# Kernel tuning notes

Hardware: AMD Instinct MI355X
Metric: run time of the kernel (lower is better)

The kernel has to match this reference:

```python
import jax, jax.numpy as jnp
import numpy as np
import math

D_MODEL = 1024
NUM_HEADS = 16
HEAD_DIM = D_MODEL // NUM_HEADS
ROPE_THETA = 10000.0
MAX_SEQ_LEN = 4096


def setup_inputs() -> dict:
    key = jax.random.key(0)
    ks = jax.random.split(key, 6)
    sigma = math.sqrt(2.0 / (D_MODEL + D_MODEL))
    def w(k):
        # trunc_normal within [-3sigma, 3sigma] ~ approximate with clipped normal
        return jnp.clip(sigma * jax.random.normal(k, (D_MODEL, D_MODEL), dtype=jnp.float32), -3 * sigma, 3 * sigma)
    x = jax.random.normal(ks[0], (2, 2048, D_MODEL), dtype=jnp.float32)
    token_positions = jnp.arange(2048, dtype=jnp.int64 if jax.config.jax_enable_x64 else jnp.int32)
    return {
        "x": x,
        "wq": w(ks[1]),
        "wk": w(ks[2]),
        "wv": w(ks[3]),
        "wo": w(ks[4]),
        "token_positions": token_positions,
    }


def _rope(t, positions):
    # t: (B, H, S, head_dim); positions: (S,)
    half = HEAD_DIM // 2
    inv_freq = 1.0 / (ROPE_THETA ** (jnp.arange(0, HEAD_DIM, 2, dtype=jnp.float32) / HEAD_DIM))  # (half,)
    freqs = positions.astype(jnp.float32)[:, None] * inv_freq[None, :]  # (S, half)
    cos = jnp.cos(freqs)
    sin = jnp.sin(freqs)
    t_even = t[..., ::2]   # (B,H,S,half)
    t_odd = t[..., 1::2]
    rot_even = t_even * cos - t_odd * sin
    rot_odd = t_even * sin + t_odd * cos
    return jnp.stack([rot_even, rot_odd], axis=-1).reshape(t.shape)


def reference(x, wq, wk, wv, wo, token_positions):
    B, S, _ = x.shape
    def split_heads(t):
        return t.reshape(B, S, NUM_HEADS, HEAD_DIM).transpose(0, 2, 1, 3)  # (B,H,S,Dh)
    q = split_heads(jnp.einsum('bsd,ed->bse', x, wq))
    k = split_heads(jnp.einsum('bsd,ed->bse', x, wk))
    v = split_heads(jnp.einsum('bsd,ed->bse', x, wv))
    q = _rope(q, token_positions)
    k = _rope(k, token_positions)
    scores = jnp.einsum('bhqd,bhkd->bhqk', q, k) / math.sqrt(HEAD_DIM)
    causal = jnp.tril(jnp.ones((S, S), dtype=bool))
    scores = jnp.where(causal, scores, -jnp.inf)
    probs = jax.nn.softmax(scores, axis=-1)
    out = jnp.einsum('bhqk,bhkd->bhqd', probs, v)  # (B,H,S,Dh)
    out = out.transpose(0, 2, 1, 3).reshape(B, S, D_MODEL)
    return jnp.einsum('bsd,ed->bse', out, wo)
```

## Files before the change

### kernel.cpp

```cpp
#include <hip/hip_runtime.h>
#include <hip/hip_bf16.h>


#define D_MODEL 1024
#define NHEADS  16
#define HDIM    64
#define SEQ     2048
#define BATCH   2

typedef unsigned short u16;
typedef __bf16 bf16x8_t __attribute__((ext_vector_type(8)));
typedef float  f32x4_t  __attribute__((ext_vector_type(4)));

__device__ __forceinline__ u16 f2bf(float f) {
    union { __hip_bfloat16 h; u16 u; } cv;
    cv.h = __float2bfloat16(f);
    return cv.u;
}

__device__ __forceinline__ unsigned pk2(float x, float y) {
    union { __hip_bfloat162 h; unsigned u; } cv;
    cv.h = __float22bfloat162_rn(make_float2(x, y));
    return cv.u;
}

__device__ __forceinline__ uint4 pack8(float4 a, float4 b) {
    uint4 u;
    u.x = pk2(a.x, a.y);
    u.y = pk2(a.z, a.w);
    u.z = pk2(b.x, b.y);
    u.w = pk2(b.z, b.w);
    return u;
}

__device__ __forceinline__ bf16x8_t frag_ld(const u16* p) {
    union { uint4 u; bf16x8_t v; } t;
    t.u = *(const uint4*)p;
    return t.v;
}

__device__ __forceinline__ void acc8(uint4 u, float* a) {
    a[0] += __uint_as_float(u.x << 16); a[1] += __uint_as_float(u.x & 0xffff0000u);
    a[2] += __uint_as_float(u.y << 16); a[3] += __uint_as_float(u.y & 0xffff0000u);
    a[4] += __uint_as_float(u.z << 16); a[5] += __uint_as_float(u.z & 0xffff0000u);
    a[6] += __uint_as_float(u.w << 16); a[7] += __uint_as_float(u.w & 0xffff0000u);
}

__device__ __forceinline__ void dma16(const u16* g, u16* l) {
    __builtin_amdgcn_global_load_lds(
        (const __attribute__((address_space(1))) void*)g,
        (__attribute__((address_space(3))) void*)l, 16, 0, 0);
}

__global__ __launch_bounds__(256) void conv_bf16_kernel(
    const float* __restrict__ X, const float* __restrict__ Wq,
    const float* __restrict__ Wk, const float* __restrict__ Wv,
    const float* __restrict__ Wo, u16* __restrict__ Xbf, u16* __restrict__ Wbf)
{
    const size_t gid = (size_t)blockIdx.x * 256 + threadIdx.x;
    const float* src;
    u16* dst;
    size_t off;
    if (gid < (1u << 19)) {
        src = X; dst = Xbf; off = gid;
    } else {
        size_t g = gid - (1u << 19);
        const int wsel = (int)(g >> 17);
        g &= (1u << 17) - 1;
        src = (wsel == 0) ? Wq : (wsel == 1) ? Wk : (wsel == 2) ? Wv : Wo;
        dst = Wbf + ((size_t)wsel << 20);
        off = g;
    }
    const float4 a = *(const float4*)(src + off * 8);
    const float4 b = *(const float4*)(src + off * 8 + 4);
    *(uint4*)(dst + off * 8) = pack8(a, b);
}

__global__ __launch_bounds__(256) void qkv_rope_kernel(
    const u16* __restrict__ Xbf, const u16* __restrict__ Wbf,
    const int* __restrict__ pos,
    u16* __restrict__ Qo, u16* __restrict__ Ko, u16* __restrict__ Vt)
{
    __shared__ __align__(16) u16 smem[16896];
    u16* As = smem;
    u16* Bs = smem + 8192;

    const int tid = threadIdx.x;
    const int m0 = blockIdx.y * 128;
    const int nv = blockIdx.x * 128;
    const int which = nv >> 10;
    const int nbase = nv & 1023;
    const u16* __restrict__ Wsrc = Wbf + ((size_t)which << 20);

    const int w = tid >> 6, L = tid & 63, quad = L >> 4, colL = L & 15;
    const int mw = (w & 1) * 64, nw = (w >> 1) * 64;

    const int lrow = L >> 3;
    const int lchk = (L & 7) ^ lrow;
    const u16* ag = Xbf + (size_t)(m0 + 32 * w + lrow) * D_MODEL + lchk * 8;
    const u16* bg = Wsrc + (size_t)(nbase + 32 * w + lrow) * D_MODEL + lchk * 8;
    u16* al = As + (32 * w) * 64;
    u16* bl = Bs + (32 * w) * 64;

    f32x4_t acc[4][4];
    #pragma unroll
    for (int i = 0; i < 4; ++i)
        #pragma unroll
        for (int j = 0; j < 4; ++j) acc[i][j] = (f32x4_t){0.f, 0.f, 0.f, 0.f};

    for (int k0 = 0; k0 < D_MODEL; k0 += 64) {
        __syncthreads();
        #pragma unroll
        for (int j = 0; j < 4; ++j) {
            dma16(ag + (size_t)j * 8 * D_MODEL + k0, al + j * 512);
            dma16(bg + (size_t)j * 8 * D_MODEL + k0, bl + j * 512);
        }
        __syncthreads();
        #pragma unroll
        for (int kb = 0; kb < 2; ++kb) {
            const int ch = ((kb * 4 + quad) ^ (colL & 7)) * 8;
            bf16x8_t af[4], bf[4];
            #pragma unroll
            for (int t = 0; t < 4; ++t) {
                af[t] = frag_ld(As + (mw + t * 16 + colL) * 64 + ch);
                bf[t] = frag_ld(Bs + (nw + t * 16 + colL) * 64 + ch);
            }
            #pragma unroll
            for (int mt = 0; mt < 4; ++mt)
                #pragma unroll
                for (int nt = 0; nt < 4; ++nt)
                    acc[mt][nt] = __builtin_amdgcn_mfma_f32_16x16x32_bf16(
                        af[mt], bf[nt], acc[mt][nt], 0, 0, 0);
        }
    }

    __syncthreads();
    u16 (*Ts)[132] = (u16(*)[132])smem;

    const float C0 = 0.14391156831212787f;
    if (which < 2) {
        const float oscale = (which == 0) ? 0.18033688011112042f : 1.0f;
        float invf[4], sgn[4];
        #pragma unroll
        for (int nt = 0; nt < 4; ++nt) {
            const int n = nbase + nw + nt * 16 + colL;
            const int dd = n & 63;
            invf[nt] = __expf(-(float)(dd & 62) * C0);
            sgn[nt] = (dd & 1) ? 1.0f : -1.0f;
        }
        #pragma unroll
        for (int mt = 0; mt < 4; ++mt) {
            #pragma unroll
            for (int r = 0; r < 4; ++r) {
                const int ml = mw + mt * 16 + quad * 4 + r;
                const int ss = (m0 + ml) & 2047;
                const float p = (float)pos[ss];
                #pragma unroll
                for (int nt = 0; nt < 4; ++nt) {
                    const float v = acc[mt][nt][r];
                    const float partner = __shfl_xor(v, 1);
                    float sn, cs;
                    __sincosf(p * invf[nt], &sn, &cs);
                    Ts[ml][nw + nt * 16 + colL] =
                        f2bf((v * cs + sgn[nt] * sn * partner) * oscale);
                }
            }
        }
    } else {
        #pragma unroll
        for (int mt = 0; mt < 4; ++mt)
            #pragma unroll
            for (int nt = 0; nt < 4; ++nt)
                #pragma unroll
                for (int r = 0; r < 4; ++r)
                    Ts[nw + nt * 16 + colL][mw + mt * 16 + quad * 4 + r] = f2bf(acc[mt][nt][r]);
    }
    __syncthreads();

    const int rr0 = tid >> 4;
    const int cc8 = (tid & 15) * 8;
    if (which < 2) {
        u16* __restrict__ dst = (which == 0) ? Qo : Ko;
        #pragma unroll
        for (int it = 0; it < 8; ++it) {
            const int ml = rr0 + it * 16;
            const int m = m0 + ml, bb = m >> 11, ss = m & 2047;
            const int n = nbase + cc8, h = n >> 6, d = n & 63;
            *(uint4*)&dst[((size_t)(bb * NHEADS + h) * SEQ + ss) * HDIM + d] =
                *(const uint4*)&Ts[ml][cc8];
        }
    } else {
        const int bb = m0 >> 11, ss0 = (m0 & 2047) + cc8;
        #pragma unroll
        for (int it = 0; it < 8; ++it) {
            const int nl = rr0 + it * 16;
            const int n = nbase + nl, h = n >> 6, d = n & 63;
            *(uint4*)&Vt[((size_t)(bb * NHEADS + h) * HDIM + d) * SEQ + ss0] =
                *(const uint4*)&Ts[nl][cc8];
        }
    }
}

__global__ __launch_bounds__(256) void attn_kernel(
    const u16* __restrict__ Q, const u16* __restrict__ K,
    const u16* __restrict__ Vt, u16* __restrict__ Opart, float* __restrict__ Lpart)
{
    __shared__ __align__(16) u16 Qs[64][72];
    __shared__ __align__(16) u16 Ks[64][72];
    __shared__ __align__(16) u16 Vs[64][72];
    __shared__ __align__(16) u16 Ps[4][16][72];

    const int tid = threadIdx.x;
    const int slot = 79 - (int)blockIdx.x;
    const int g = (slot >= 48) ? 3 : (slot >= 24) ? 2 : (slot >= 8) ? 1 : 0;
    const int t0 = slot - 4 * g * (g + 1);
    const int rr = t0 / (g + 1);
    const int s  = t0 - rr * (g + 1);
    const int qt = 8 * g + rr;

    const int hh = blockIdx.y, bb = blockIdx.z;
    const size_t bh = ((size_t)bb * NHEADS + hh) * (SEQ * HDIM);
    const int q0 = qt * 64;
    const int kt0 = s * 8;
    const int ktend = min(kt0 + 8, qt + 1);
    const size_t gslot = ((size_t)(bb * NHEADS + hh) * 80 + slot);

    const int w = tid >> 6, L = tid & 63, quad = L >> 4, colL = L & 15;
    const int srow = tid >> 2, sc = (tid & 3) * 16;

    {
        const u16* qp = Q + bh + (size_t)(q0 + srow) * HDIM + sc;
        *(uint4*)&Qs[srow][sc]     = *(const uint4*)qp;
        *(uint4*)&Qs[srow][sc + 8] = *(const uint4*)(qp + 8);
    }

    float lsum = 0.f;
    f32x4_t O[4];
    #pragma unroll
    for (int dt = 0; dt < 4; ++dt) O[dt] = (f32x4_t){0.f, 0.f, 0.f, 0.f};

    const u16* kp = K + bh + (size_t)(kt0 * 64 + srow) * HDIM + sc;
    const u16* vp = Vt + bh + (size_t)srow * SEQ + kt0 * 64 + sc;
    uint4 kv0 = *(const uint4*)kp;
    uint4 kv1 = *(const uint4*)(kp + 8);
    uint4 vv0 = *(const uint4*)vp;
    uint4 vv1 = *(const uint4*)(vp + 8);

    for (int kt = kt0; kt < ktend; ++kt) {
        __syncthreads();
        *(uint4*)&Ks[srow][sc]     = kv0;
        *(uint4*)&Ks[srow][sc + 8] = kv1;
        *(uint4*)&Vs[srow][sc]     = vv0;
        *(uint4*)&Vs[srow][sc + 8] = vv1;
        if (kt + 1 < ktend) {
            const int k1 = (kt + 1) * 64;
            const u16* kpn = K + bh + (size_t)(k1 + srow) * HDIM + sc;
            kv0 = *(const uint4*)kpn;
            kv1 = *(const uint4*)(kpn + 8);
            const u16* vpn = Vt + bh + (size_t)srow * SEQ + k1 + sc;
            vv0 = *(const uint4*)vpn;
            vv1 = *(const uint4*)(vpn + 8);
        }
        __syncthreads();

        const bool diag = (kt == qt);
        const int ntmax = diag ? w : 3;

        f32x4_t S[4];
        #pragma unroll
        for (int nt = 0; nt < 4; ++nt) S[nt] = (f32x4_t){0.f, 0.f, 0.f, 0.f};
        #pragma unroll
        for (int kb = 0; kb < 2; ++kb) {
            const bf16x8_t aq = frag_ld(&Qs[w * 16 + colL][kb * 32 + quad * 8]);
            for (int nt = 0; nt <= ntmax; ++nt) {
                const bf16x8_t bk = frag_ld(&Ks[nt * 16 + colL][kb * 32 + quad * 8]);
                S[nt] = __builtin_amdgcn_mfma_f32_16x16x32_bf16(bk, aq, S[nt], 0, 0, 0);
            }
        }

        if (!diag) {
            #pragma unroll
            for (int nt = 0; nt < 4; ++nt) {
                const float p0 = __builtin_amdgcn_exp2f(S[nt][0]);
                const float p1 = __builtin_amdgcn_exp2f(S[nt][1]);
                const float p2 = __builtin_amdgcn_exp2f(S[nt][2]);
                const float p3 = __builtin_amdgcn_exp2f(S[nt][3]);
                lsum += (p0 + p1) + (p2 + p3);
                uint2 pw;
                pw.x = pk2(p0, p1);
                pw.y = pk2(p2, p3);
                *(uint2*)&Ps[w][colL][nt * 16 + quad * 4] = pw;
            }
        } else {
            const int qrel = w * 16 + colL;
            #pragma unroll
            for (int nt = 0; nt < 4; ++nt) {
                float p0 = 0.f, p1 = 0.f, p2 = 0.f, p3 = 0.f;
                if (nt <= ntmax) {
                    const int krel = nt * 16 + quad * 4;
                    p0 = (krel + 0 <= qrel) ? __builtin_amdgcn_exp2f(S[nt][0]) : 0.f;
                    p1 = (krel + 1 <= qrel) ? __builtin_amdgcn_exp2f(S[nt][1]) : 0.f;
                    p2 = (krel + 2 <= qrel) ? __builtin_amdgcn_exp2f(S[nt][2]) : 0.f;
                    p3 = (krel + 3 <= qrel) ? __builtin_amdgcn_exp2f(S[nt][3]) : 0.f;
                }
                lsum += (p0 + p1) + (p2 + p3);
                uint2 pw;
                pw.x = pk2(p0, p1);
                pw.y = pk2(p2, p3);
                *(uint2*)&Ps[w][colL][nt * 16 + quad * 4] = pw;
            }
        }

        asm volatile("s_waitcnt lgkmcnt(0)" ::: "memory");

        const int kbmax = diag ? (w >> 1) : 1;
        #pragma unroll
        for (int kb = 0; kb < 2; ++kb) {
            if (kb > kbmax) break;
            const bf16x8_t ap = frag_ld(&Ps[w][colL][kb * 32 + quad * 8]);
            #pragma unroll
            for (int dt = 0; dt < 4; ++dt) {
                const bf16x8_t bv = frag_ld(&Vs[dt * 16 + colL][kb * 32 + quad * 8]);
                O[dt] = __builtin_amdgcn_mfma_f32_16x16x32_bf16(ap, bv, O[dt], 0, 0, 0);
            }
        }
    }

    {
        float sm = lsum;
        sm += __shfl_xor(sm, 16);
        sm += __shfl_xor(sm, 32);
        if (quad == 0)
            Lpart[gslot * 64 + 16 * w + colL] = sm;
    }

    #pragma unroll
    for (int dt = 0; dt < 4; ++dt)
        #pragma unroll
        for (int r = 0; r < 4; ++r)
            Ps[w][quad * 4 + r][dt * 16 + colL] = f2bf(O[dt][r]);
    asm volatile("s_waitcnt lgkmcnt(0)" ::: "memory");
    #pragma unroll
    for (int p = 0; p < 2; ++p) {
        const int rowl = (L >> 3) + 8 * p;
        const int c8 = (L & 7) * 8;
        *(uint4*)&Opart[gslot * 4096 + (size_t)(16 * w + rowl) * 64 + c8] =
            *(const uint4*)&Ps[w][rowl][c8];
    }
}

__global__ __launch_bounds__(256) void combine_kernel(
    const u16* __restrict__ Opart, const float* __restrict__ Lpart,
    u16* __restrict__ AO)
{
    const int qt = blockIdx.x, hh = blockIdx.y, bb = blockIdx.z;
    const int g = qt >> 3;
    const int nsplit = g + 1;
    const int base = 4 * g * (g + 1) + (qt & 7) * (g + 1);
    const int t = threadIdx.x;
    const int q = t >> 2, dg = (t & 3) * 16;
    const size_t slot0 = (size_t)(bb * NHEADS + hh) * 80 + base;

    float acc[16];
    #pragma unroll
    for (int i = 0; i < 16; ++i) acc[i] = 0.f;
    float l = 0.f;
    for (int s = 0; s < nsplit; ++s) {
        const size_t gs = slot0 + s;
        l += Lpart[gs * 64 + q];
        const u16* op = Opart + gs * 4096 + (size_t)q * 64 + dg;
        acc8(*(const uint4*)op, acc);
        acc8(*(const uint4*)(op + 8), acc + 8);
    }
    const float inv = 1.0f / l;
    uint4 o0, o1;
    o0.x = pk2(acc[0] * inv, acc[1] * inv);  o0.y = pk2(acc[2] * inv, acc[3] * inv);
    o0.z = pk2(acc[4] * inv, acc[5] * inv);  o0.w = pk2(acc[6] * inv, acc[7] * inv);
    o1.x = pk2(acc[8] * inv, acc[9] * inv);  o1.y = pk2(acc[10] * inv, acc[11] * inv);
    o1.z = pk2(acc[12] * inv, acc[13] * inv); o1.w = pk2(acc[14] * inv, acc[15] * inv);
    u16* dst = AO + ((size_t)bb * SEQ + qt * 64 + q) * D_MODEL + hh * HDIM + dg;
    *(uint4*)dst = o0;
    *(uint4*)(dst + 8) = o1;
}

__global__ __launch_bounds__(256) void out_proj_kernel(
    const u16* __restrict__ A, const u16* __restrict__ Wob, float* __restrict__ Out)
{
    __shared__ __align__(16) u16 smem[16384];
    u16* As = smem;
    u16* Bs = smem + 8192;

    const int tid = threadIdx.x;
    const int m0 = blockIdx.y * 128;
    const int n0 = blockIdx.x * 128;

    const int w = tid >> 6, L = tid & 63, quad = L >> 4, colL = L & 15;
    const int mw = (w & 1) * 64, nw = (w >> 1) * 64;

    const int lrow = L >> 3;
    const int lchk = (L & 7) ^ lrow;
    const u16* ag = A + (size_t)(m0 + 32 * w + lrow) * D_MODEL + lchk * 8;
    const u16* bg = Wob + (size_t)(n0 + 32 * w + lrow) * D_MODEL + lchk * 8;
    u16* al = As + (32 * w) * 64;
    u16* bl = Bs + (32 * w) * 64;

    f32x4_t acc[4][4];
    #pragma unroll
    for (int i = 0; i < 4; ++i)
        #pragma unroll
        for (int j = 0; j < 4; ++j) acc[i][j] = (f32x4_t){0.f, 0.f, 0.f, 0.f};

    for (int k0 = 0; k0 < D_MODEL; k0 += 64) {
        __syncthreads();
        #pragma unroll
        for (int j = 0; j < 4; ++j) {
            dma16(ag + (size_t)j * 8 * D_MODEL + k0, al + j * 512);
            dma16(bg + (size_t)j * 8 * D_MODEL + k0, bl + j * 512);
        }
        __syncthreads();
        #pragma unroll
        for (int kb = 0; kb < 2; ++kb) {
            const int ch = ((kb * 4 + quad) ^ (colL & 7)) * 8;
            bf16x8_t af[4], bf[4];
            #pragma unroll
            for (int t = 0; t < 4; ++t) {
                af[t] = frag_ld(As + (mw + t * 16 + colL) * 64 + ch);
                bf[t] = frag_ld(Bs + (nw + t * 16 + colL) * 64 + ch);
            }
            #pragma unroll
            for (int mt = 0; mt < 4; ++mt)
                #pragma unroll
                for (int nt = 0; nt < 4; ++nt)
                    acc[mt][nt] = __builtin_amdgcn_mfma_f32_16x16x32_bf16(
                        af[mt], bf[nt], acc[mt][nt], 0, 0, 0);
        }
    }

    #pragma unroll
    for (int mt = 0; mt < 4; ++mt)
        #pragma unroll
        for (int nt = 0; nt < 4; ++nt)
            #pragma unroll
            for (int r = 0; r < 4; ++r) {
                const int m = m0 + mw + mt * 16 + quad * 4 + r;
                const int n = n0 + nw + nt * 16 + colL;
                Out[(size_t)m * D_MODEL + n] = acc[mt][nt][r];
            }
}

extern "C" void kernel_launch(void* const* d_in, const int* in_sizes, int n_in,
                              void* d_out, int out_size, void* d_ws, size_t ws_size,
                              hipStream_t stream) {
    const float* x  = (const float*)d_in[0];
    const float* wq = (const float*)d_in[1];
    const float* wk = (const float*)d_in[2];
    const float* wv = (const float*)d_in[3];
    const float* wo = (const float*)d_in[4];
    const int* pos  = (const int*)d_in[5];
    float* out = (float*)d_out;

    const size_t NELEM = (size_t)BATCH * NHEADS * SEQ * HDIM;
    u16* Qw  = (u16*)d_ws;
    u16* Kw  = Qw + NELEM;
    u16* Vtw = Kw + NELEM;
    u16* AOw = Vtw + NELEM;
    u16* Xbf = AOw;
    u16* Wbf = AOw + NELEM;
    u16* Opart = Wbf + NELEM;
    float* Lpart = (float*)(Opart + (size_t)2560 * 4096);

    conv_bf16_kernel<<<4096, 256, 0, stream>>>(x, wq, wk, wv, wo, Xbf, Wbf);
    qkv_rope_kernel<<<dim3(24, 32), 256, 0, stream>>>(Xbf, Wbf, pos, Qw, Kw, Vtw);
    attn_kernel<<<dim3(80, NHEADS, BATCH), 256, 0, stream>>>(Qw, Kw, Vtw, Opart, Lpart);
    combine_kernel<<<dim3(32, NHEADS, BATCH), 256, 0, stream>>>(Opart, Lpart, AOw);
    out_proj_kernel<<<dim3(8, 32), 256, 0, stream>>>(AOw, Wbf + 3 * (1u << 20), out);
}
```

Measured before the change: 212.2 us.

## Load Q/K/V MFMA fragments directly from global memory, removing LDS staging and barriers

The attention kernel no longer stages Q, K and V tiles through shared memory. Each lane now loads its MFMA operand fragments straight from global memory (cached in L1/L2), which removes both per-iteration __syncthreads and the LDS writes and reads. The cost is redundant global loads across the four waves, since each wave now fetches the full K and V tiles. The explicit register prefetch of the next tile is also gone, so global-load latency is exposed unless waves overlap.

After: 296.5 us. 1.4x slower.

```diff
diff --git a/kernel.cpp b/kernel.cpp
--- a/kernel.cpp
+++ b/kernel.cpp
@@ -36,6 +36,12 @@
 __device__ __forceinline__ bf16x8_t frag_ld(const u16* p) {
     union { uint4 u; bf16x8_t v; } t;
     t.u = *(const uint4*)p;
+    return t.v;
+}
+
+__device__ __forceinline__ bf16x8_t frag_cast(uint4 u) {
+    union { uint4 u; bf16x8_t v; } t;
+    t.u = u;
     return t.v;
 }
 
@@ -205,9 +211,6 @@
     const u16* __restrict__ Q, const u16* __restrict__ K,
     const u16* __restrict__ Vt, u16* __restrict__ Opart, float* __restrict__ Lpart)
 {
-    __shared__ __align__(16) u16 Qs[64][72];
-    __shared__ __align__(16) u16 Ks[64][72];
-    __shared__ __align__(16) u16 Vs[64][72];
     __shared__ __align__(16) u16 Ps[4][16][72];
 
     const int tid = threadIdx.x;
@@ -226,55 +229,53 @@
     const size_t gslot = ((size_t)(bb * NHEADS + hh) * 80 + slot);
 
     const int w = tid >> 6, L = tid & 63, quad = L >> 4, colL = L & 15;
-    const int srow = tid >> 2, sc = (tid & 3) * 16;
-
-    {
-        const u16* qp = Q + bh + (size_t)(q0 + srow) * HDIM + sc;
-        *(uint4*)&Qs[srow][sc]     = *(const uint4*)qp;
-        *(uint4*)&Qs[srow][sc + 8] = *(const uint4*)(qp + 8);
-    }
+
+    const u16* qp = Q + bh + (size_t)(q0 + w * 16 + colL) * HDIM + quad * 8;
+    const bf16x8_t aq0 = frag_ld(qp);
+    const bf16x8_t aq1 = frag_ld(qp + 32);
+
+    const u16* kbase = K + bh + (size_t)(kt0 * 64 + colL) * HDIM + quad * 8;
+    const u16* vbase = Vt + bh + (size_t)colL * SEQ + kt0 * 64 + quad * 8;
 
     float lsum = 0.f;
     f32x4_t O[4];
     #pragma unroll
     for (int dt = 0; dt < 4; ++dt) O[dt] = (f32x4_t){0.f, 0.f, 0.f, 0.f};
 
-    const u16* kp = K + bh + (size_t)(kt0 * 64 + srow) * HDIM + sc;
-    const u16* vp = Vt + bh + (size_t)srow * SEQ + kt0 * 64 + sc;
-    uint4 kv0 = *(const uint4*)kp;
-    uint4 kv1 = *(const uint4*)(kp + 8);
-    uint4 vv0 = *(const uint4*)vp;
-    uint4 vv1 = *(const uint4*)(vp + 8);
-
     for (int kt = kt0; kt < ktend; ++kt) {
-        __syncthreads();
-        *(uint4*)&Ks[srow][sc]     = kv0;
-        *(uint4*)&Ks[srow][sc + 8] = kv1;
-        *(uint4*)&Vs[srow][sc]     = vv0;
-        *(uint4*)&Vs[srow][sc + 8] = vv1;
-        if (kt + 1 < ktend) {
-            const int k1 = (kt + 1) * 64;
-            const u16* kpn = K + bh + (size_t)(k1 + srow) * HDIM + sc;
-            kv0 = *(const uint4*)kpn;
-            kv1 = *(const uint4*)(kpn + 8);
-            const u16* vpn = Vt + bh + (size_t)srow * SEQ + k1 + sc;
-            vv0 = *(const uint4*)vpn;
-            vv1 = *(const uint4*)(vpn + 8);
-        }
-        __syncthreads();
-
         const bool diag = (kt == qt);
         const int ntmax = diag ? w : 3;
+        const int kbmax = diag ? (w >> 1) : 1;
+
+        uint4 kf0[4], kf1[4];
+        #pragma unroll
+        for (int nt = 0; nt < 4; ++nt) {
+            if (nt <= ntmax) {
+                kf0[nt] = *(const uint4*)(kbase + nt * 1024);
+                kf1[nt] = *(const uint4*)(kbase + nt * 1024 + 32);
+            }
+        }
 
         f32x4_t S[4];
         #pragma unroll
         for (int nt = 0; nt < 4; ++nt) S[nt] = (f32x4_t){0.f, 0.f, 0.f, 0.f};
         #pragma unroll
+        for (int nt = 0; nt < 4; ++nt) {
+            if (nt <= ntmax) {
+                S[nt] = __builtin_amdgcn_mfma_f32_16x16x32_bf16(
+                    frag_cast(kf0[nt]), aq0, S[nt], 0, 0, 0);
+                S[nt] = __builtin_amdgcn_mfma_f32_16x16x32_bf16(
+                    frag_cast(kf1[nt]), aq1, S[nt], 0, 0, 0);
+            }
+        }
+
+        uint4 vf[2][4];
+        #pragma unroll
         for (int kb = 0; kb < 2; ++kb) {
-            const bf16x8_t aq = frag_ld(&Qs[w * 16 + colL][kb * 32 + quad * 8]);
-            for (int nt = 0; nt <= ntmax; ++nt) {
-                const bf16x8_t bk = frag_ld(&Ks[nt * 16 + colL][kb * 32 + quad * 8]);
-                S[nt] = __builtin_amdgcn_mfma_f32_16x16x32_bf16(bk, aq, S[nt], 0, 0, 0);
+            if (kb <= kbmax) {
+                #pragma unroll
+                for (int dt = 0; dt < 4; ++dt)
+                    vf[kb][dt] = *(const uint4*)(vbase + (size_t)dt * (16 * SEQ) + kb * 32);
             }
         }
 
@@ -313,17 +314,19 @@
 
         asm volatile("s_waitcnt lgkmcnt(0)" ::: "memory");
 
-        const int kbmax = diag ? (w >> 1) : 1;
         #pragma unroll
         for (int kb = 0; kb < 2; ++kb) {
-            if (kb > kbmax) break;
-            const bf16x8_t ap = frag_ld(&Ps[w][colL][kb * 32 + quad * 8]);
-            #pragma unroll
-            for (int dt = 0; dt < 4; ++dt) {
-                const bf16x8_t bv = frag_ld(&Vs[dt * 16 + colL][kb * 32 + quad * 8]);
-                O[dt] = __builtin_amdgcn_mfma_f32_16x16x32_bf16(ap, bv, O[dt], 0, 0, 0);
-            }
-        }
+            if (kb <= kbmax) {
+                const bf16x8_t ap = frag_ld(&Ps[w][colL][kb * 32 + quad * 8]);
+                #pragma unroll
+                for (int dt = 0; dt < 4; ++dt)
+                    O[dt] = __builtin_amdgcn_mfma_f32_16x16x32_bf16(
+                        ap, frag_cast(vf[kb][dt]), O[dt], 0, 0, 0);
+            }
+        }
+
+        kbase += 64 * HDIM;
+        vbase += 64;
     }
 
     {
```
